# Optimization experiments

Measured on AMD Instinct MI355X. Metric: run time of the kernel, lower is better.

The kernel has to match this reference:

```python
import jax, jax.numpy as jnp
import numpy as np

HEADS = 4


def setup_inputs() -> dict:
    key = jax.random.key(0)
    kx, kqkv, kbq, ko, kbo = jax.random.split(key, 5)
    B, C, H, W = 4, 256, 64, 64
    x = jax.random.normal(kx, (B, C, H, W), dtype=jnp.float32)
    # torch nn.Linear stores weight as [out_features, in_features]
    w_qkv = jax.random.normal(kqkv, (3 * C, C), dtype=jnp.float32) * (1.0 / np.sqrt(C))
    b_qkv = jax.random.normal(kbq, (3 * C,), dtype=jnp.float32) * 0.02
    w_o = jax.random.normal(ko, (C, C), dtype=jnp.float32) * (1.0 / np.sqrt(C))
    b_o = jax.random.normal(kbo, (C,), dtype=jnp.float32) * 0.02
    return {"x": x, "w_qkv": w_qkv, "b_qkv": b_qkv, "w_o": w_o, "b_o": b_o}


def reference(x, w_qkv, b_qkv, w_o, b_o):
    B, C, H, W = x.shape
    S = H * W
    hd = C // HEADS
    # (B, C, H, W) -> (B, S, C)
    xt = x.reshape(B, C, S).transpose(0, 2, 1)
    qkv = xt @ w_qkv.T + b_qkv                      # (B, S, 3C)
    q, k, v = jnp.split(qkv, 3, axis=-1)
    def to_heads(t):
        return t.reshape(B, S, HEADS, hd).transpose(0, 2, 1, 3)  # (B, h, S, hd)
    q, k, v = to_heads(q), to_heads(k), to_heads(v)
    scores = jnp.einsum('bhqd,bhkd->bhqk', q, k) / jnp.sqrt(jnp.float32(hd))
    attn = jax.nn.softmax(scores, axis=-1)          # dropout inactive (eval)
    out = jnp.einsum('bhqk,bhkd->bhqd', attn, v)    # (B, h, S, hd)
    out = out.transpose(0, 2, 1, 3).reshape(B, S, C)
    y = out @ w_o.T + b_o                            # (B, S, C)
    y = y.reshape(B, H, W, C).transpose(0, 3, 1, 2)  # (B, C, H, W)
    return y
```

## Files before the change

kernel.cpp:

```cpp
#include <hip/hip_runtime.h>
#include <stdint.h>

#define DI __device__ __forceinline__

typedef __attribute__((ext_vector_type(8))) __bf16 bf16x8;
typedef __attribute__((ext_vector_type(8))) unsigned short u16x8;
typedef __attribute__((ext_vector_type(4))) float f32x4;
typedef __attribute__((ext_vector_type(4))) uint32_t u32x4;
typedef unsigned short u16;

constexpr int Bb = 4, Cc = 256, Ss = 4096, HD = 64;
constexpr int ELEMS = Bb * Cc * Ss;

DI float bf2f(u16 h) { union { unsigned u; float f; } x; x.u = ((unsigned)h) << 16; return x.f; }
DI u16 f2bf(float f) {
  union { float f; unsigned u; } x; x.f = f;
  return (u16)((x.u + 0x7FFFu + ((x.u >> 16) & 1u)) >> 16);
}
DI uint32_t pack2bf_trunc(float a, float b) {
  union { float f; uint32_t u; } xa, xb;
  xa.f = a; xb.f = b;
  return __builtin_amdgcn_perm(xb.u, xa.u, 0x07060302u);
}
DI float truncbf(float f) {
  union { float f; unsigned u; } x; x.f = f; x.u &= 0xFFFF0000u; return x.f;
}
DI bf16x8 ldfrag(const u16* p) { return __builtin_bit_cast(bf16x8, *(const u16x8*)p); }

DI void g2l16(const u16* g, u16* l) {
  __builtin_amdgcn_global_load_lds((const __attribute__((address_space(1))) uint32_t*)(const void*)g,
                                   (__attribute__((address_space(3))) uint32_t*)(void*)l, 16, 0, 0);
}

__global__ __launch_bounds__(256) void k_transpose(const float* __restrict__ x, u16* __restrict__ xt,
                                                   const float* __restrict__ wq, const float* __restrict__ wo,
                                                   u16* __restrict__ wqb, u16* __restrict__ wob) {
  __shared__ u16 T[64][72];
  const int st = blockIdx.x, ct = blockIdx.y, b = blockIdx.z;
  const int tid = threadIdx.x;
  {
    int flat = blockIdx.x + 64 * blockIdx.y + 256 * blockIdx.z;
    int widx = flat * 256 + tid;
    if (widx < 196608) wqb[widx] = f2bf(wq[widx]);
    else wob[widx - 196608] = f2bf(wo[widx - 196608]);
  }
#pragma unroll
  for (int e = 0; e < 2; e++) {
    int ss = tid + e * 256;
    int r = ss >> 3, seg = ss & 7;
    size_t base = ((size_t)(b * Cc + ct * 64 + r) << 12) + st * 64 + seg * 8;
    u16x8 t;
#pragma unroll
    for (int j = 0; j < 8; j++) t[j] = f2bf(x[base + j]);
    *(u16x8*)&T[r][(seg ^ ((r >> 3) & 7)) * 8] = t;
  }
  __syncthreads();
#pragma unroll
  for (int e = 0; e < 2; e++) {
    int ss = tid + e * 256;
    int sr = ss >> 3, cseg = ss & 7;
    u16x8 o;
#pragma unroll
    for (int j = 0; j < 8; j++) {
      int row = cseg * 8 + j;
      o[j] = T[row][(((sr >> 3) ^ cseg) * 8) + (sr & 7)];
    }
    *(u16x8*)(xt + ((size_t)(b * Ss + st * 64 + sr) << 8) + ct * 64 + cseg * 8) = o;
  }
}

DI void stage_tile(const u16* __restrict__ src, int pitch, int r0, int k0, u16 (*dst)[40], int tid) {
#pragma unroll
  for (int e = 0; e < 2; e++) {
    int c = tid + e * 256;
    int row = c >> 2, seg = c & 3;
    u16x8 t = *(const u16x8*)(src + (size_t)(r0 + row) * pitch + k0 + seg * 8);
    *(u16x8*)&dst[row][seg * 8] = t;
  }
}

__global__ __launch_bounds__(256) void k_qkv(const u16* __restrict__ xt, const u16* __restrict__ w,
                                             const float* __restrict__ bias,
                                             u16* __restrict__ q, u16* __restrict__ kk_, u16* __restrict__ vv_) {
  __shared__ u16 As[128][40], Bs[128][40];
  const int tid = threadIdx.x;
  const int wv = tid >> 6, lane = tid & 63;
  const int wm = wv >> 1, wn = wv & 1;
  const int lr = lane & 15, quad = lane >> 4;
  const int r0 = blockIdx.x * 128;
  const int j0 = blockIdx.y * 128;
  f32x4 acc[4][4] = {};
  for (int k0 = 0; k0 < 256; k0 += 32) {
    __syncthreads();
    stage_tile(xt, 256, r0, k0, As, tid);
    stage_tile(w, 256, j0, k0, Bs, tid);
    __syncthreads();
    bf16x8 a[4], b[4];
#pragma unroll
    for (int mt = 0; mt < 4; mt++) a[mt] = ldfrag(&As[wm * 64 + mt * 16 + lr][quad * 8]);
#pragma unroll
    for (int nt = 0; nt < 4; nt++) b[nt] = ldfrag(&Bs[wn * 64 + nt * 16 + lr][quad * 8]);
#pragma unroll
    for (int mt = 0; mt < 4; mt++)
#pragma unroll
      for (int nt = 0; nt < 4; nt++)
        acc[mt][nt] = __builtin_amdgcn_mfma_f32_16x16x32_bf16(a[mt], b[nt], acc[mt][nt], 0, 0, 0);
  }
#pragma unroll
  for (int nt = 0; nt < 4; nt++) {
    int j = j0 + wn * 64 + nt * 16 + lr;
    float bj = bias[j];
    int part = j >> 8, cc = j & 255, head = cc >> 6, d = cc & 63;
    u16* outp = (part == 0) ? q : (part == 1) ? kk_ : vv_;
    float sc = (part == 0) ? 0.18033688f : 1.0f;
#pragma unroll
    for (int mt = 0; mt < 4; mt++)
#pragma unroll
      for (int rg = 0; rg < 4; rg++) {
        int row = r0 + wm * 64 + mt * 16 + quad * 4 + rg;
        int b_ = row >> 12, s = row & 4095;
        outp[((size_t)((b_ * 4 + head) * Ss + s) << 6) + d] = f2bf((acc[mt][nt][rg] + bj) * sc);
      }
  }
}

__global__ __launch_bounds__(256) void k_vt(const u16* __restrict__ v, u16* __restrict__ vt) {
  __shared__ u16 T[64][72];
  const int chunk = blockIdx.x, bh = blockIdx.y;
  const int tid = threadIdx.x;
#pragma unroll
  for (int e = 0; e < 2; e++) {
    int row = (tid >> 3) + e * 32, seg = tid & 7;
    *(u16x8*)&T[row][(seg ^ ((row >> 3) & 7)) * 8] =
        *(const u16x8*)(v + ((size_t)(bh * Ss + chunk * 64 + row) << 6) + seg * 8);
  }
  __syncthreads();
#pragma unroll
  for (int e = 0; e < 2; e++) {
    int d = (tid >> 3) + e * 32, seg = tid & 7;
    u16x8 o;
#pragma unroll
    for (int j = 0; j < 8; j++) {
      int slot = seg * 8 + j;
      int t = (((slot >> 5) & 1) << 1) | ((slot >> 2) & 1);
      int w6 = t * 16 + (((slot >> 3) & 3) << 2) + (slot & 3);
      o[j] = T[w6][(((d >> 3) ^ ((w6 >> 3) & 7)) * 8) + (d & 7)];
    }
    *(u16x8*)(vt + ((size_t)(bh * 64 + d) << 12) + chunk * 64 + seg * 8) = o;
  }
}

__global__ __launch_bounds__(256, 3) void k_attn(const u16* __restrict__ Q, const u16* __restrict__ K,
                                                 const u16* __restrict__ VT, u16* __restrict__ AO,
                                                 u16* __restrict__ AOP, float* __restrict__ lpart,
                                                 int nsplit) {
  __shared__ u16 Kl[2][64][64];
  __shared__ u16 Vl[2][64][64];
  const int tid = threadIdx.x;
  const int wv = tid >> 6, lane = tid & 63;
  const int lr = lane & 15, quad = lane >> 4;
  const int bh = blockIdx.y;
  const int b_ = bh >> 2, head = bh & 3;
  const int qbase = blockIdx.x * 128 + wv * 32;
  const int sp = blockIdx.z;
  const int nchunk = 64 / nsplit, kcg0 = sp * nchunk;
  const u16* Qh = Q + (size_t)bh * Ss * HD;
  const u16* Kh = K + (size_t)bh * Ss * HD;
  const u16* Vh = VT + (size_t)bh * HD * Ss;

  bf16x8 qb[2][2];
#pragma unroll
  for (int nt = 0; nt < 2; nt++)
#pragma unroll
    for (int ks = 0; ks < 2; ks++)
      qb[nt][ks] = ldfrag(Qh + (size_t)(qbase + nt * 16 + lr) * HD + ks * 32 + quad * 8);

  f32x4 O[2][4] = {};
  float lsum[2] = {0.f, 0.f};

  const int lrow = lane >> 3;
  const int lseg = ((lane & 7) ^ lrow) * 8;
  const int kd0 = wv * 16 + lrow;
  const u16* pK0 = Kh + ((size_t)(kcg0 * 64 + kd0) << 6) + lseg;
  const u16* pK1 = pK0 + (8 << 6);
  const u16* pV0 = Vh + ((size_t)kd0 << 12) + kcg0 * 64 + lseg;
  const u16* pV1 = pV0 + ((size_t)8 << 12);
  auto stage = [&](int buf) {
    g2l16(pK0, &Kl[buf][wv * 16][0]);
    g2l16(pK1, &Kl[buf][wv * 16 + 8][0]);
    g2l16(pV0, &Vl[buf][wv * 16][0]);
    g2l16(pV1, &Vl[buf][wv * 16 + 8][0]);
    pK0 += 4096; pK1 += 4096; pV0 += 64; pV1 += 64;
  };

  stage(0);
  __syncthreads();

  for (int kc = 0; kc < nchunk; kc++) {
    const int cur = kc & 1;
    if (kc + 1 < nchunk) stage(cur ^ 1);

    u32x4 pa[2][2];
#pragma unroll
    for (int t = 0; t < 4; t++) {
      const int krow = t * 16 + lr;
      bf16x8 ka0 = ldfrag(&Kl[cur][krow][(quad ^ (lr & 7)) * 8]);
      bf16x8 ka1 = ldfrag(&Kl[cur][krow][((4 + quad) ^ (lr & 7)) * 8]);
      f32x4 St[2] = {};
      __builtin_amdgcn_s_setprio(1);
#pragma unroll
      for (int nt = 0; nt < 2; nt++)
        St[nt] = __builtin_amdgcn_mfma_f32_16x16x32_bf16(ka0, qb[nt][0], St[nt], 0, 0, 0);
#pragma unroll
      for (int nt = 0; nt < 2; nt++)
        St[nt] = __builtin_amdgcn_mfma_f32_16x16x32_bf16(ka1, qb[nt][1], St[nt], 0, 0, 0);
      __builtin_amdgcn_s_setprio(0);
      const int h = t >> 1, k2 = (t & 1) * 2;
#pragma unroll
      for (int nt = 0; nt < 2; nt++) {
        float p0 = __builtin_amdgcn_exp2f(St[nt][0]);
        float p1 = __builtin_amdgcn_exp2f(St[nt][1]);
        float p2 = __builtin_amdgcn_exp2f(St[nt][2]);
        float p3 = __builtin_amdgcn_exp2f(St[nt][3]);
        pa[h][nt][k2] = pack2bf_trunc(p0, p1);
        pa[h][nt][k2 + 1] = pack2bf_trunc(p2, p3);
        lsum[nt] += (truncbf(p0) + truncbf(p1)) + (truncbf(p2) + truncbf(p3));
      }
    }
#pragma unroll
    for (int h = 0; h < 2; h++)
#pragma unroll
      for (int dt = 0; dt < 4; dt++) {
        bf16x8 vb = ldfrag(&Vl[cur][dt * 16 + lr][((h * 4 + quad) ^ (lr & 7)) * 8]);
        __builtin_amdgcn_s_setprio(1);
#pragma unroll
        for (int mt = 0; mt < 2; mt++)
          O[mt][dt] = __builtin_amdgcn_mfma_f32_16x16x32_bf16(
              __builtin_bit_cast(bf16x8, pa[h][mt]), vb, O[mt][dt], 0, 0, 0);
        __builtin_amdgcn_s_setprio(0);
      }
    __syncthreads();
  }

  float lfull[2];
#pragma unroll
  for (int nt = 0; nt < 2; nt++) {
    float r = lsum[nt] + __shfl_xor(lsum[nt], 16, 64);
    r += __shfl_xor(r, 32, 64);
    lfull[nt] = r;
  }
  float lval[2][4];
#pragma unroll
  for (int mt = 0; mt < 2; mt++)
#pragma unroll
    for (int rg = 0; rg < 4; rg++)
      lval[mt][rg] = __shfl(lfull[mt], quad * 4 + rg, 64);

  u16* dst = (nsplit == 1) ? AO : (AOP + (size_t)sp * ELEMS);
  if (nsplit > 1 && lr == 0) {
    float* lp = lpart + (size_t)sp * (16 * Ss) + bh * Ss;
#pragma unroll
    for (int mt = 0; mt < 2; mt++)
#pragma unroll
      for (int rg = 0; rg < 4; rg++) lp[qbase + mt * 16 + quad * 4 + rg] = lval[mt][rg];
  }
#pragma unroll
  for (int mt = 0; mt < 2; mt++)
#pragma unroll
    for (int rg = 0; rg < 4; rg++) {
      float inv = 1.0f / lval[mt][rg];
      int s = qbase + mt * 16 + quad * 4 + rg;
#pragma unroll
      for (int dt = 0; dt < 4; dt++)
        dst[((size_t)(b_ * Ss + s) << 8) + head * 64 + dt * 16 + lr] = f2bf(O[mt][dt][rg] * inv);
    }
}

__global__ __launch_bounds__(256) void k_oproj(const u16* __restrict__ wo, const u16* __restrict__ ao,
                                               const u16* __restrict__ AOP, const float* __restrict__ lpart,
                                               const float* __restrict__ bo, float* __restrict__ y, int nsplit) {
  __shared__ u16 As[128][40], Bs[128][40];
  const int tid = threadIdx.x;
  const int wv = tid >> 6, lane = tid & 63;
  const int wm = wv >> 1, wn = wv & 1;
  const int lr = lane & 15, quad = lane >> 4;
  const int n0 = blockIdx.x * 128;
  const int m0 = blockIdx.y * 128;
  f32x4 acc[4][4] = {};
  for (int k0 = 0; k0 < 256; k0 += 32) {
    __syncthreads();
    stage_tile(wo, 256, m0, k0, As, tid);
#pragma unroll
    for (int e = 0; e < 2; e++) {
      int c = tid + e * 256;
      int row = c >> 2, seg = c & 3;
      int bs = n0 + row, cc = k0 + seg * 8;
      u16x8 t;
      if (nsplit == 1) {
        t = *(const u16x8*)(ao + ((size_t)bs << 8) + cc);
      } else {
        int b = bs >> 12, s = bs & 4095, head = cc >> 6;
        int li = (b * 4 + head) * Ss + s;
        float accv[8] = {0.f, 0.f, 0.f, 0.f, 0.f, 0.f, 0.f, 0.f};
        float lsum = 0.f;
        for (int spl = 0; spl < nsplit; spl++) {
          float l = lpart[(size_t)spl * (16 * Ss) + li];
          u16x8 a = *(const u16x8*)(AOP + (size_t)spl * ELEMS + ((size_t)bs << 8) + cc);
          lsum += l;
#pragma unroll
          for (int i = 0; i < 8; i++) accv[i] += l * bf2f(a[i]);
        }
        float inv = 1.0f / lsum;
#pragma unroll
        for (int i = 0; i < 8; i++) t[i] = f2bf(accv[i] * inv);
      }
      *(u16x8*)&Bs[row][seg * 8] = t;
    }
    __syncthreads();
    bf16x8 a[4], b[4];
#pragma unroll
    for (int mt = 0; mt < 4; mt++) a[mt] = ldfrag(&As[wm * 64 + mt * 16 + lr][quad * 8]);
#pragma unroll
    for (int nt = 0; nt < 4; nt++) b[nt] = ldfrag(&Bs[wn * 64 + nt * 16 + lr][quad * 8]);
#pragma unroll
    for (int mt = 0; mt < 4; mt++)
#pragma unroll
      for (int nt = 0; nt < 4; nt++)
        acc[mt][nt] = __builtin_amdgcn_mfma_f32_16x16x32_bf16(a[mt], b[nt], acc[mt][nt], 0, 0, 0);
  }
#pragma unroll
  for (int mt = 0; mt < 4; mt++)
#pragma unroll
    for (int rg = 0; rg < 4; rg++) {
      int c = m0 + wm * 64 + mt * 16 + quad * 4 + rg;
      float bc = bo[c];
#pragma unroll
      for (int nt = 0; nt < 4; nt++) {
        int col = n0 + wn * 64 + nt * 16 + lr;
        int b_ = col >> 12, s = col & 4095;
        y[((size_t)(b_ * Cc + c) << 12) + s] = acc[mt][nt][rg] + bc;
      }
    }
}

extern "C" void kernel_launch(void* const* d_in, const int* in_sizes, int n_in,
                              void* d_out, int out_size, void* d_ws, size_t ws_size,
                              hipStream_t stream) {
  const float* x = (const float*)d_in[0];
  const float* w_qkv = (const float*)d_in[1];
  const float* b_qkv = (const float*)d_in[2];
  const float* w_o = (const float*)d_in[3];
  const float* b_o = (const float*)d_in[4];
  float* y = (float*)d_out;
  u16* ws = (u16*)d_ws;
  u16* xt = ws;
  u16* q = ws + (size_t)ELEMS;
  u16* k = ws + (size_t)2 * ELEMS;
  u16* vt = ws + (size_t)3 * ELEMS;
  u16* ao = xt;
  u16* wqb = ws + (size_t)4 * ELEMS;
  u16* wob = wqb + 196608;
  const size_t Wu16 = (size_t)4 * ELEMS + 262144;
  auto need = [&](int n) { return (Wu16 + (size_t)n * ELEMS) * 2 + (size_t)n * 16 * Ss * 4; };
  const int nsplit = (ws_size >= need(2)) ? 2 : 1;
  u16* aop = ws + Wu16;
  u16* v = aop;
  float* lpart = (float*)(aop + (size_t)nsplit * ELEMS);

  k_transpose<<<dim3(64, 4, 4), 256, 0, stream>>>(x, xt, w_qkv, w_o, wqb, wob);
  k_qkv<<<dim3(128, 6), 256, 0, stream>>>(xt, wqb, b_qkv, q, k, v);
  k_vt<<<dim3(64, 16), 256, 0, stream>>>(v, vt);
  k_attn<<<dim3(32, 16, nsplit), 256, 0, stream>>>(q, k, vt, ao, aop, lpart, nsplit);
  k_oproj<<<dim3(128, 2), 256, 0, stream>>>(wob, ao, aop, lpart, b_o, y, nsplit);
}
```

Before: 193.6 us.

## Use 512-thread attention blocks and compute softmax row sums via MFMA

Doubles the attention workgroup to 8 waves covering 256 queries, so each staged K/V chunk in LDS is shared by twice as many queries and each thread issues half as many global-to-LDS loads. The row-sum of the probabilities is now computed by an extra MFMA against a vector of bf16 ones instead of scalar truncation adds plus cross-lane shuffles. This removes VALU work and the final shuffle reduction but adds matrix instructions, and the larger blocks give fewer workgroups and may limit occupancy.

```diff
diff --git a/kernel.cpp b/kernel.cpp
--- a/kernel.cpp
+++ b/kernel.cpp
@@ -21,9 +21,6 @@
   union { float f; uint32_t u; } xa, xb;
   xa.f = a; xb.f = b;
   return __builtin_amdgcn_perm(xb.u, xa.u, 0x07060302u);
-}
-DI float truncbf(float f) {
-  union { float f; unsigned u; } x; x.f = f; x.u &= 0xFFFF0000u; return x.f;
 }
 DI bf16x8 ldfrag(const u16* p) { return __builtin_bit_cast(bf16x8, *(const u16x8*)p); }
 
@@ -150,7 +147,7 @@
   }
 }
 
-__global__ __launch_bounds__(256, 3) void k_attn(const u16* __restrict__ Q, const u16* __restrict__ K,
+__global__ __launch_bounds__(512, 4) void k_attn(const u16* __restrict__ Q, const u16* __restrict__ K,
                                                  const u16* __restrict__ VT, u16* __restrict__ AO,
                                                  u16* __restrict__ AOP, float* __restrict__ lpart,
                                                  int nsplit) {
@@ -161,7 +158,7 @@
   const int lr = lane & 15, quad = lane >> 4;
   const int bh = blockIdx.y;
   const int b_ = bh >> 2, head = bh & 3;
-  const int qbase = blockIdx.x * 128 + wv * 32;
+  const int qbase = blockIdx.x * 256 + wv * 32;
   const int sp = blockIdx.z;
   const int nchunk = 64 / nsplit, kcg0 = sp * nchunk;
   const u16* Qh = Q + (size_t)bh * Ss * HD;
@@ -175,22 +172,22 @@
     for (int ks = 0; ks < 2; ks++)
       qb[nt][ks] = ldfrag(Qh + (size_t)(qbase + nt * 16 + lr) * HD + ks * 32 + quad * 8);
 
+  u16x8 ov;
+#pragma unroll
+  for (int j = 0; j < 8; j++) ov[j] = 0x3F80;
+  const bf16x8 ones = __builtin_bit_cast(bf16x8, ov);
+
   f32x4 O[2][4] = {};
-  float lsum[2] = {0.f, 0.f};
-
-  const int lrow = lane >> 3;
-  const int lseg = ((lane & 7) ^ lrow) * 8;
-  const int kd0 = wv * 16 + lrow;
-  const u16* pK0 = Kh + ((size_t)(kcg0 * 64 + kd0) << 6) + lseg;
-  const u16* pK1 = pK0 + (8 << 6);
-  const u16* pV0 = Vh + ((size_t)kd0 << 12) + kcg0 * 64 + lseg;
-  const u16* pV1 = pV0 + ((size_t)8 << 12);
+  f32x4 lacc[2] = {};
+
+  const int srow = wv * 8 + (lane >> 3);
+  const int sseg = ((lane & 7) ^ (lane >> 3)) * 8;
+  const u16* pK = Kh + ((size_t)(kcg0 * 64 + srow) << 6) + sseg;
+  const u16* pV = Vh + ((size_t)srow << 12) + kcg0 * 64 + sseg;
   auto stage = [&](int buf) {
-    g2l16(pK0, &Kl[buf][wv * 16][0]);
-    g2l16(pK1, &Kl[buf][wv * 16 + 8][0]);
-    g2l16(pV0, &Vl[buf][wv * 16][0]);
-    g2l16(pV1, &Vl[buf][wv * 16 + 8][0]);
-    pK0 += 4096; pK1 += 4096; pV0 += 64; pV1 += 64;
+    g2l16(pK, &Kl[buf][wv * 8][0]);
+    g2l16(pV, &Vl[buf][wv * 8][0]);
+    pK += 4096; pV += 64;
   };
 
   stage(0);
@@ -224,11 +221,10 @@
         float p3 = __builtin_amdgcn_exp2f(St[nt][3]);
         pa[h][nt][k2] = pack2bf_trunc(p0, p1);
         pa[h][nt][k2 + 1] = pack2bf_trunc(p2, p3);
-        lsum[nt] += (truncbf(p0) + truncbf(p1)) + (truncbf(p2) + truncbf(p3));
-      }
-    }
-#pragma unroll
-    for (int h = 0; h < 2; h++)
+      }
+    }
+#pragma unroll
+    for (int h = 0; h < 2; h++) {
 #pragma unroll
       for (int dt = 0; dt < 4; dt++) {
         bf16x8 vb = ldfrag(&Vl[cur][dt * 16 + lr][((h * 4 + quad) ^ (lr & 7)) * 8]);
@@ -239,22 +235,13 @@
               __builtin_bit_cast(bf16x8, pa[h][mt]), vb, O[mt][dt], 0, 0, 0);
         __builtin_amdgcn_s_setprio(0);
       }
-    __syncthreads();
-  }
-
-  float lfull[2];
-#pragma unroll
-  for (int nt = 0; nt < 2; nt++) {
-    float r = lsum[nt] + __shfl_xor(lsum[nt], 16, 64);
-    r += __shfl_xor(r, 32, 64);
-    lfull[nt] = r;
-  }
-  float lval[2][4];
-#pragma unroll
-  for (int mt = 0; mt < 2; mt++)
-#pragma unroll
-    for (int rg = 0; rg < 4; rg++)
-      lval[mt][rg] = __shfl(lfull[mt], quad * 4 + rg, 64);
+#pragma unroll
+      for (int mt = 0; mt < 2; mt++)
+        lacc[mt] = __builtin_amdgcn_mfma_f32_16x16x32_bf16(
+            __builtin_bit_cast(bf16x8, pa[h][mt]), ones, lacc[mt], 0, 0, 0);
+    }
+    __syncthreads();
+  }
 
   u16* dst = (nsplit == 1) ? AO : (AOP + (size_t)sp * ELEMS);
   if (nsplit > 1 && lr == 0) {
@@ -262,13 +249,13 @@
 #pragma unroll
     for (int mt = 0; mt < 2; mt++)
 #pragma unroll
-      for (int rg = 0; rg < 4; rg++) lp[qbase + mt * 16 + quad * 4 + rg] = lval[mt][rg];
+      for (int rg = 0; rg < 4; rg++) lp[qbase + mt * 16 + quad * 4 + rg] = lacc[mt][rg];
   }
 #pragma unroll
   for (int mt = 0; mt < 2; mt++)
 #pragma unroll
     for (int rg = 0; rg < 4; rg++) {
-      float inv = 1.0f / lval[mt][rg];
+      float inv = 1.0f / lacc[mt][rg];
       int s = qbase + mt * 16 + quad * 4 + rg;
 #pragma unroll
       for (int dt = 0; dt < 4; dt++)
@@ -370,6 +357,6 @@
   k_transpose<<<dim3(64, 4, 4), 256, 0, stream>>>(x, xt, w_qkv, w_o, wqb, wob);
   k_qkv<<<dim3(128, 6), 256, 0, stream>>>(xt, wqb, b_qkv, q, k, v);
   k_vt<<<dim3(64, 16), 256, 0, stream>>>(v, vt);
-  k_attn<<<dim3(32, 16, nsplit), 256, 0, stream>>>(q, k, vt, ao, aop, lpart, nsplit);
+  k_attn<<<dim3(16, 16, nsplit), 512, 0, stream>>>(q, k, vt, ao, aop, lpart, nsplit);
   k_oproj<<<dim3(128, 2), 256, 0, stream>>>(wob, ao, aop, lpart, b_o, y, nsplit);
 }
```

New measurement: 179.0 us. 1.08x faster.
